# Performance work log

Hardware: AMD Instinct MI355X
Metric: run time of the kernel (lower is better)

Reference implementation:

```python
import jax, jax.numpy as jnp
import numpy as np

B, T, N, L, D, F = 8, 1024, 512, 4096, 512, 64  # batch, target, nodes, leaves, d_model, d_feature
BR = L // N  # branching factor: leaves per node


def setup_inputs() -> dict:
    key = jax.random.key(0)
    ks = jax.random.split(key, 10)
    s = 0.02
    return {
        "root": jax.random.normal(ks[0], (B, 1, F), dtype=jnp.float32),
        "node": jax.random.normal(ks[1], (B, N, D), dtype=jnp.float32),
        "leaf": jax.random.normal(ks[2], (B, L, D), dtype=jnp.float32),
        "target": jax.random.normal(ks[3], (B, T, D), dtype=jnp.float32),
        "Wq": jax.random.normal(ks[4], (D, F), dtype=jnp.float32) * s,
        "bq": jnp.zeros((F,), dtype=jnp.float32),
        "Wk": jax.random.normal(ks[5], (D, F), dtype=jnp.float32) * s,
        "bk": jnp.zeros((F,), dtype=jnp.float32),
        "Wv": jax.random.normal(ks[6], (D, F), dtype=jnp.float32) * s,
        "bv": jnp.zeros((F,), dtype=jnp.float32),
        "Wagg": jax.random.normal(ks[7], (D, 1), dtype=jnp.float32) * s,
        "bagg": jnp.zeros((1,), dtype=jnp.float32),
    }


def reference(root, node, leaf, target, Wq, bq, Wk, bk, Wv, bv, Wagg, bagg):
    # Shared DecoderLinear projections (same weights used for node and leaf).
    q = target @ Wq + bq                      # [B,T,F]
    node_k = node @ Wk + bk                   # [B,N,F]
    node_v = node @ Wv + bv                   # [B,N,F]
    leaf_k = leaf @ Wk + bk                   # [B,L,F]
    leaf_v = leaf @ Wv + bv                   # [B,L,F]

    scale = 1.0 / jnp.sqrt(jnp.asarray(F, dtype=q.dtype))
    # Dual-key attention weights (no value-matmul inside attention()).
    Aqn = jax.nn.softmax(jnp.einsum('btf,bnf->btn', q, node_k) * scale, axis=-1)  # [B,T,N]
    Aql = jax.nn.softmax(jnp.einsum('btf,blf->btl', q, leaf_k) * scale, axis=-1)  # [B,T,L]

    # Tree interpolation: each leaf mixes root, its parent node value, and itself.
    node_rep = jnp.repeat(node_v, BR, axis=1)               # [B,L,F]
    interp = (root + node_rep + leaf_v) / 3.0               # [B,L,F]

    # Upward cumulative aggregation: suffix mean along the leaf dimension.
    rev_cumsum = jnp.cumsum(interp[:, ::-1, :], axis=1)[:, ::-1, :]  # [B,L,F]
    counts = (L - jnp.arange(L)).astype(interp.dtype)[None, :, None]
    upward = rev_cumsum / counts                                     # [B,L,F]

    # Weighted aggregation: learned softmax weights over each node's leaf group.
    w = jax.nn.softmax((leaf @ Wagg + bagg).reshape(B, N, BR), axis=-1)   # [B,N,BR]
    node_hat = jnp.einsum('bnc,bncf->bnf', w, upward.reshape(B, N, BR, F))  # [B,N,F]

    # Fused cat + matmul + softmax.
    A = jnp.concatenate([Aqn, Aql], axis=-1)          # [B,T,N+L]
    V = jnp.concatenate([node_hat, leaf_v], axis=-2)  # [B,N+L,F]
    return jax.nn.softmax(jnp.einsum('btm,bmf->btf', A, V), axis=-1)  # [B,T,F]
```

## Files before the change

kernel.cpp:

```cpp
#include <hip/hip_runtime.h>

#define B_ 8
#define T_ 1024
#define N_ 512
#define L_ 4096
#define D_ 512
#define F_ 64
#define SLICES 8
#define TPS 9
#define KSTR 72
#define XSTR 264

typedef __attribute__((ext_vector_type(8))) short short8;
typedef __attribute__((ext_vector_type(4))) float f32x4;

__device__ __forceinline__ unsigned short f2bf(float x){
    unsigned u = __builtin_bit_cast(unsigned, x);
    u += 0x7FFFu + ((u >> 16) & 1u);
    return (unsigned short)(u >> 16);
}
__device__ __forceinline__ unsigned pack_bf(float lo, float hi){
    return (unsigned)f2bf(lo) | ((unsigned)f2bf(hi) << 16);
}
__device__ __forceinline__ float bf2f(unsigned short s){
    return __builtin_bit_cast(float, ((unsigned)s) << 16);
}
__device__ __forceinline__ short8 frag_from4(unsigned d0, unsigned d1, unsigned d2, unsigned d3){
    union { unsigned u[4]; short8 s; } t;
    t.u[0] = d0; t.u[1] = d1; t.u[2] = d2; t.u[3] = d3;
    return t.s;
}

__global__ __launch_bounds__(64)
void prep_kernel(const float* __restrict__ Wq, const float* __restrict__ bq,
                 const float* __restrict__ Wk, const float* __restrict__ bk,
                 const float* __restrict__ Wv, const float* __restrict__ bv,
                 unsigned short* __restrict__ Wq_t, unsigned short* __restrict__ Wkv_t,
                 float* __restrict__ bq_s, float* __restrict__ bkv)
{
    const int n = blockIdx.x;
    const int lane = threadIdx.x;
    if (n == 192) {
        bq_s[lane]   = bq[lane] * 0.125f;
        bkv[lane]    = bk[lane];
        bkv[64+lane] = bv[lane];
        return;
    }
    const int d0 = lane * 8;
    unsigned short t[8];
    if (n < 64) {
        #pragma unroll
        for (int j = 0; j < 8; ++j) t[j] = f2bf(Wq[(size_t)(d0+j)*F_ + n] * 0.125f);
        *(uint4*)&Wq_t[(size_t)n*D_ + d0] = make_uint4(
            (unsigned)t[0]|((unsigned)t[1]<<16), (unsigned)t[2]|((unsigned)t[3]<<16),
            (unsigned)t[4]|((unsigned)t[5]<<16), (unsigned)t[6]|((unsigned)t[7]<<16));
    } else {
        const int nn  = n - 64;
        const float* W = (nn < 64) ? Wk : Wv;
        const int col = nn & 63;
        #pragma unroll
        for (int j = 0; j < 8; ++j) t[j] = f2bf(W[(size_t)(d0+j)*F_ + col]);
        *(uint4*)&Wkv_t[(size_t)nn*D_ + d0] = make_uint4(
            (unsigned)t[0]|((unsigned)t[1]<<16), (unsigned)t[2]|((unsigned)t[3]<<16),
            (unsigned)t[4]|((unsigned)t[5]<<16), (unsigned)t[6]|((unsigned)t[7]<<16));
    }
}

template<int MODE>
__device__ __forceinline__ void proj_body(
    int r0, unsigned short* Xs, unsigned short* Ws, unsigned short* Vt_lds,
    const float* __restrict__ X,
    const unsigned short* __restrict__ Wt,
    const float* __restrict__ bias,
    const float* __restrict__ Wagg, const float* __restrict__ bagg,
    unsigned short* __restrict__ outK, float* __restrict__ outVf,
    unsigned short* __restrict__ outVt, float* __restrict__ outAgg)
{
    constexpr int NPASS = (MODE == 0) ? 1 : 2;
    const int tid = threadIdx.x;
    const int l = tid & 63, c = l & 15, h = l >> 4;
    const int w  = tid >> 6;
    const int nt = w & 3;
    const int m  = w >> 2;

    f32x4 acc0 = {0,0,0,0};
    f32x4 acc1 = {0,0,0,0};
    float pa = 0.f;

    #pragma unroll
    for (int kc = 0; kc < 2; ++kc) {
        #pragma unroll
        for (int j = 0; j < 4; ++j) {
            const int s = tid + j * 1024;
            const int row = s >> 6, col = s & 63;
            const float4 v = *(const float4*)(X + (size_t)(r0+row)*D_ + kc*256 + col*4);
            *(uint2*)&Xs[row*XSTR + col*4] =
                make_uint2(pack_bf(v.x, v.y), pack_bf(v.z, v.w));
        }
        {
            const int r = tid >> 4, ch = tid & 15;
            #pragma unroll
            for (int j = 0; j < 2; ++j) {
                const int u = ch + j*16;
                *(uint4*)&Ws[r*XSTR + u*8] =
                    *(const uint4*)(Wt + (size_t)r*D_ + kc*256 + u*8);
            }
        }
        __syncthreads();

        #pragma unroll
        for (int kk = 0; kk < 8; ++kk) {
            const short8 bfr = *(const short8*)&Ws[(16*nt + c)*XSTR + kk*32 + 8*h];
            const short8 af  = *(const short8*)&Xs[(16*m  + c)*XSTR + kk*32 + 8*h];
            acc0 = __builtin_amdgcn_mfma_f32_16x16x32_bf16(af, bfr, acc0, 0,0,0);
        }
        __syncthreads();

        if constexpr (NPASS == 2) {
            {
                const int r = tid >> 4, ch = tid & 15;
                #pragma unroll
                for (int j = 0; j < 2; ++j) {
                    const int u = ch + j*16;
                    *(uint4*)&Ws[r*XSTR + u*8] =
                        *(const uint4*)(Wt + (size_t)(64 + r)*D_ + kc*256 + u*8);
                }
            }
            __syncthreads();
            #pragma unroll
            for (int kk = 0; kk < 8; ++kk) {
                const short8 bfr = *(const short8*)&Ws[(16*nt + c)*XSTR + kk*32 + 8*h];
                const short8 af  = *(const short8*)&Xs[(16*m  + c)*XSTR + kk*32 + 8*h];
                acc1 = __builtin_amdgcn_mfma_f32_16x16x32_bf16(af, bfr, acc1, 0,0,0);
            }
            if constexpr (MODE == 2) {
                const int row = tid >> 4, qd = tid & 15;
                const unsigned short* xr = &Xs[row*XSTR + qd*16];
                const float* wr = Wagg + kc*256 + qd*16;
                #pragma unroll
                for (int j = 0; j < 2; ++j) {
                    const short8 xv = *(const short8*)(xr + j*8);
                    const float4 wa0 = *(const float4*)(wr + j*8);
                    const float4 wa1 = *(const float4*)(wr + j*8 + 4);
                    pa += bf2f((unsigned short)xv[0])*wa0.x + bf2f((unsigned short)xv[1])*wa0.y
                        + bf2f((unsigned short)xv[2])*wa0.z + bf2f((unsigned short)xv[3])*wa0.w
                        + bf2f((unsigned short)xv[4])*wa1.x + bf2f((unsigned short)xv[5])*wa1.y
                        + bf2f((unsigned short)xv[6])*wa1.z + bf2f((unsigned short)xv[7])*wa1.w;
                }
            }
            __syncthreads();
        }
    }

    {
        const float bc0 = bias[16*nt + c];
        #pragma unroll
        for (int r = 0; r < 4; ++r) {
            const int row = r0 + 16*m + 4*h + r;
            outK[(size_t)row*F_ + 16*nt + c] = f2bf(acc0[r] + bc0);
        }
    }
    if constexpr (NPASS == 2) {
        const float bc1 = bias[64 + 16*nt + c];
        #pragma unroll
        for (int r = 0; r < 4; ++r) {
            const int row = r0 + 16*m + 4*h + r;
            const float v = acc1[r] + bc1;
            if constexpr (MODE == 1) {
                outVf[(size_t)row*F_ + 16*nt + c] = v;
            } else {
                Vt_lds[(16*nt + c)*72 + 16*m + 4*h + r] = f2bf(v);
            }
        }
    }

    if constexpr (MODE == 2) {
        {
            const int row = tid >> 4, qd = tid & 15;
            pa += __shfl_xor(pa, 1);
            pa += __shfl_xor(pa, 2);
            pa += __shfl_xor(pa, 4);
            pa += __shfl_xor(pa, 8);
            if (qd == 0) outAgg[r0 + row] = pa + bagg[0];
        }
        __syncthreads();
        {
            const int f = tid >> 4, seg = tid & 15;
            const int b = r0 >> 12, l0 = r0 & (L_ - 1);
            const uint2 a0 = *(const uint2*)&Vt_lds[f*72 + seg*4];
            *(uint2*)(outVt + ((size_t)(b*F_ + f))*L_ + l0 + seg*4) = a0;
        }
    }
}

__global__ __launch_bounds__(1024, 8)
void proj_all(const float* __restrict__ target, const float* __restrict__ node,
              const float* __restrict__ leaf,
              const unsigned short* __restrict__ Wq_t,
              const unsigned short* __restrict__ Wkv_t,
              const float* __restrict__ bq_s, const float* __restrict__ bkv,
              const float* __restrict__ Wagg, const float* __restrict__ bagg,
              unsigned short* __restrict__ q_bf, unsigned short* __restrict__ nk_bf,
              float* __restrict__ node_v, unsigned short* __restrict__ lk_bf,
              unsigned short* __restrict__ lvt, float* __restrict__ agg)
{
    __shared__ unsigned short Xs[64 * XSTR];
    __shared__ unsigned short Ws[64 * XSTR];
    __shared__ unsigned short Vt_lds[64 * 72];
    const int blk = blockIdx.x;
    if (blk < 512) {
        proj_body<2>(blk*64, Xs, Ws, Vt_lds, leaf, Wkv_t, bkv, Wagg, bagg,
                     lk_bf, nullptr, lvt, agg);
    } else if (blk < 640) {
        proj_body<0>((blk-512)*64, Xs, Ws, Vt_lds, target, Wq_t, bq_s, nullptr, nullptr,
                     q_bf, nullptr, nullptr, nullptr);
    } else {
        proj_body<1>((blk-640)*64, Xs, Ws, Vt_lds, node, Wkv_t, bkv, nullptr, nullptr,
                     nk_bf, node_v, nullptr, nullptr);
    }
}

__global__ __launch_bounds__(256)
void scan_nh_kernel(const unsigned short* __restrict__ lvt,
                    const float* __restrict__ node_v,
                    const float* __restrict__ root,
                    const float* __restrict__ agg,
                    unsigned short* __restrict__ nh_t)
{
    const int gtid = blockIdx.x * 256 + threadIdx.x;
    const int wv   = gtid >> 6;
    const int lane = threadIdx.x & 63;
    const int b = wv >> 6;
    const int f = wv & 63;

    const unsigned short* vt = lvt + ((size_t)(b*F_ + f))*L_ + lane*64;
    const float rootf = root[b*F_ + f];
    short8 xv[8]; float nv[8]; float gv[8];
    #pragma unroll
    for (int g = 0; g < 8; ++g) {
        xv[g] = *(const short8*)(vt + g*8);
        nv[g] = node_v[((size_t)(b*N_ + lane*8 + g))*F_ + f];
        float s8 = 0.f;
        #pragma unroll
        for (int j = 0; j < 8; ++j) s8 += bf2f((unsigned short)xv[g][j]);
        gv[g] = (s8 + 8.f*(rootf + nv[g])) * (1.f/3.f);
    }

    float s[9];
    s[8] = 0.f;
    #pragma unroll
    for (int j = 7; j >= 0; --j) s[j] = s[j+1] + gv[j];

    float x = s[0];
    const float lsum = x;
    #pragma unroll
    for (int off = 1; off < 64; off <<= 1) {
        float t = __shfl_down(x, off);
        if (lane + off < 64) x += t;
    }
    const float excl = x - lsum;

    const float* aggb = agg + (size_t)b*L_ + lane*64;
    unsigned short out8[8];
    #pragma unroll
    for (int g = 0; g < 8; ++g) {
        const float4 a0 = *(const float4*)(aggb + g*8);
        const float4 a1 = *(const float4*)(aggb + g*8 + 4);
        const float av[8] = {a0.x,a0.y,a0.z,a0.w, a1.x,a1.y,a1.z,a1.w};
        float mx = av[0];
        #pragma unroll
        for (int cc = 1; cc < 8; ++cc) mx = fmaxf(mx, av[cc]);
        float wgt[8]; float wsum = 0.f;
        #pragma unroll
        for (int cc = 0; cc < 8; ++cc) { wgt[cc] = __expf(av[cc] - mx); wsum += wgt[cc]; }

        const float tn = excl + s[g+1];
        float run = 0.f, acc = 0.f;
        #pragma unroll
        for (int cc = 7; cc >= 0; --cc) {
            const int ll = lane*64 + g*8 + cc;
            const float interp = (rootf + nv[g] + bf2f((unsigned short)xv[g][cc])) * (1.f/3.f);
            run += interp;
            const float up = (tn + run) / (float)(L_ - ll);
            acc = fmaf(wgt[cc], up, acc);
        }
        out8[g] = f2bf(acc / wsum);
    }
    *(uint4*)&nh_t[((size_t)(b*F_ + f))*N_ + lane*8] = *(const uint4*)out8;
}

__global__ __launch_bounds__(512, 4)
void attn_kernel(const unsigned short* __restrict__ qb,
                 const unsigned short* __restrict__ nk,
                 const unsigned short* __restrict__ nht,
                 const unsigned short* __restrict__ lk,
                 const unsigned short* __restrict__ lvt,
                 unsigned short* __restrict__ pacc, float* __restrict__ pd)
{
    __shared__ unsigned short Ks[2][64*KSTR];
    __shared__ unsigned short Vt[2][64*KSTR];

    const int wg  = (blockIdx.x & 7) * 64 + (blockIdx.x >> 3);
    const int b   = wg >> 6;
    const int sl  = (wg >> 3) & 7;
    const int t0  = (wg & 7) * 128;

    const int tid = threadIdx.x;
    const int w   = tid >> 6;
    const int l   = tid & 63;
    const int c   = l & 15;
    const int h   = l >> 4;
    const int sm  = tid >> 3;
    const int sc  = tid & 7;

    const unsigned short* qrow = qb + ((size_t)(b*T_ + t0 + w*16 + c))*F_ + 8*h;
    const short8 qf0 = *(const short8*)qrow;
    const short8 qf1 = *(const short8*)(qrow + 32);

    f32x4 accN[4] = {{0,0,0,0},{0,0,0,0},{0,0,0,0},{0,0,0,0}};
    f32x4 accL[4] = {{0,0,0,0},{0,0,0,0},{0,0,0,0},{0,0,0,0}};
    float dsN = 0.f, dsL = 0.f;

    const unsigned short* Knb = nk  + (size_t)b*N_*F_;
    const unsigned short* Klb = lk  + (size_t)b*L_*F_;
    const unsigned short* Vnb = nht + (size_t)b*F_*N_;
    const unsigned short* Vlb = lvt + (size_t)b*F_*L_;

    const int ti0 = sl * TPS;

    uint4 sk0, sv0;
    auto load_tile = [&](int ti) {
        if (ti < 8) {
            sk0 = *(const uint4*)(Knb + (size_t)ti*64*F_ + sm*64 + sc*8);
            sv0 = *(const uint4*)(Vnb + (size_t)sm*N_ + ti*64 + sc*8);
        } else {
            sk0 = *(const uint4*)(Klb + (size_t)(ti-8)*64*F_ + sm*64 + sc*8);
            sv0 = *(const uint4*)(Vlb + (size_t)sm*L_ + (ti-8)*64 + sc*8);
        }
    };
    auto write_tile = [&](int pb) {
        *(uint4*)&Ks[pb][sm*KSTR + sc*8] = sk0;
        *(uint4*)&Vt[pb][sm*KSTR + sc*8] = sv0;
    };

    load_tile(ti0);
    write_tile(0);
    __syncthreads();

    const int srcA = c + 16*((2*h) & 3);
    const int srcB = c + 16*((2*h + 1) & 3);
    const int hs   = h >> 1;

    for (int i = 0; i < TPS; ++i) {
        const int  ti  = ti0 + i;
        const bool isN = ti < 8;
        const int  pb  = i & 1;
        const bool nxt = (i + 1 < TPS);
        if (nxt) load_tile(ti + 1);

        f32x4 st[4] = {{0,0,0,0},{0,0,0,0},{0,0,0,0},{0,0,0,0}};
        #pragma unroll
        for (int ss = 0; ss < 4; ++ss) {
            const short8 kf0 = *(const short8*)&Ks[pb][(16*ss + c)*KSTR + 8*h];
            st[ss] = __builtin_amdgcn_mfma_f32_16x16x32_bf16(kf0, qf0, st[ss], 0,0,0);
            const short8 kf1 = *(const short8*)&Ks[pb][(16*ss + c)*KSTR + 32 + 8*h];
            st[ss] = __builtin_amdgcn_mfma_f32_16x16x32_bf16(kf1, qf1, st[ss], 0,0,0);
        }

        unsigned pk0[4], pk1[4];
        float psum = 0.f;
        #pragma unroll
        for (int ss = 0; ss < 4; ++ss) {
            #pragma unroll
            for (int r = 0; r < 4; ++r) { st[ss][r] = __expf(st[ss][r]); psum += st[ss][r]; }
            pk0[ss] = pack_bf(st[ss][0], st[ss][1]);
            pk1[ss] = pack_bf(st[ss][2], st[ss][3]);
        }
        if (isN) dsN += psum; else dsL += psum;

        #pragma unroll
        for (int k00 = 0; k00 < 2; ++k00) {
            const unsigned d0a = __shfl(pk0[2*k00+0], srcA);
            const unsigned d0b = __shfl(pk0[2*k00+1], srcA);
            const unsigned d1a = __shfl(pk1[2*k00+0], srcA);
            const unsigned d1b = __shfl(pk1[2*k00+1], srcA);
            const unsigned d2a = __shfl(pk0[2*k00+0], srcB);
            const unsigned d2b = __shfl(pk0[2*k00+1], srcB);
            const unsigned d3a = __shfl(pk1[2*k00+0], srcB);
            const unsigned d3b = __shfl(pk1[2*k00+1], srcB);
            const short8 bp = frag_from4(hs ? d0b : d0a, hs ? d1b : d1a,
                                         hs ? d2b : d2a, hs ? d3b : d3a);
            if (isN) {
                #pragma unroll
                for (int s2 = 0; s2 < 4; ++s2) {
                    const short8 af = *(const short8*)&Vt[pb][(16*s2 + c)*KSTR + 32*k00 + 8*h];
                    accN[s2] = __builtin_amdgcn_mfma_f32_16x16x32_bf16(af, bp, accN[s2], 0,0,0);
                }
            } else {
                #pragma unroll
                for (int s2 = 0; s2 < 4; ++s2) {
                    const short8 af = *(const short8*)&Vt[pb][(16*s2 + c)*KSTR + 32*k00 + 8*h];
                    accL[s2] = __builtin_amdgcn_mfma_f32_16x16x32_bf16(af, bp, accL[s2], 0,0,0);
                }
            }
        }

        if (nxt) {
            write_tile(pb ^ 1);
            __syncthreads();
        }
    }

    dsN += __shfl_xor(dsN, 16);  dsN += __shfl_xor(dsN, 32);
    dsL += __shfl_xor(dsL, 16);  dsL += __shfl_xor(dsL, 32);

    const int gt = b*T_ + t0 + w*16 + c;
    unsigned short* baseN = pacc + (((size_t)sl*(B_*T_) + gt)*2 + 0)*F_;
    unsigned short* baseL = baseN + F_;
    #pragma unroll
    for (int s2 = 0; s2 < 4; ++s2) {
        *(unsigned*)&baseN[s2*16 + 4*h]     = pack_bf(accN[s2][0], accN[s2][1]);
        *(unsigned*)&baseN[s2*16 + 4*h + 2] = pack_bf(accN[s2][2], accN[s2][3]);
        *(unsigned*)&baseL[s2*16 + 4*h]     = pack_bf(accL[s2][0], accL[s2][1]);
        *(unsigned*)&baseL[s2*16 + 4*h + 2] = pack_bf(accL[s2][2], accL[s2][3]);
    }
    if (h == 0) {
        pd[((size_t)sl*(B_*T_) + gt)*2 + 0] = dsN;
        pd[((size_t)sl*(B_*T_) + gt)*2 + 1] = dsL;
    }
}

__global__ __launch_bounds__(256)
void combine_kernel(const unsigned short* __restrict__ pacc,
                    const float* __restrict__ pd,
                    float* __restrict__ out)
{
    const int gt = (blockIdx.x * 256 + threadIdx.x) >> 6;
    const int f  = threadIdx.x & 63;

    float aN = 0.f, aL = 0.f, dN = 0.f, dL = 0.f;
    #pragma unroll
    for (int s = 0; s < SLICES; ++s) {
        const size_t base = ((size_t)s*(B_*T_) + gt)*2;
        aN += bf2f(pacc[(base + 0)*F_ + f]);
        aL += bf2f(pacc[(base + 1)*F_ + f]);
        dN += pd[base + 0];
        dL += pd[base + 1];
    }
    float lg = aN / dN + aL / dL;
    float mx = lg;
    #pragma unroll
    for (int off = 1; off < 64; off <<= 1) mx = fmaxf(mx, __shfl_xor(mx, off));
    const float e = __expf(lg - mx);
    float ssum = e;
    #pragma unroll
    for (int off = 1; off < 64; off <<= 1) ssum += __shfl_xor(ssum, off);
    out[(size_t)gt*F_ + f] = e / ssum;
}

extern "C" void kernel_launch(void* const* d_in, const int* in_sizes, int n_in,
                              void* d_out, int out_size, void* d_ws, size_t ws_size,
                              hipStream_t stream)
{
    const float* root   = (const float*)d_in[0];
    const float* node   = (const float*)d_in[1];
    const float* leaf   = (const float*)d_in[2];
    const float* target = (const float*)d_in[3];
    const float* Wq   = (const float*)d_in[4];
    const float* bq   = (const float*)d_in[5];
    const float* Wk   = (const float*)d_in[6];
    const float* bk   = (const float*)d_in[7];
    const float* Wv   = (const float*)d_in[8];
    const float* bv   = (const float*)d_in[9];
    const float* Wagg = (const float*)d_in[10];
    const float* bagg = (const float*)d_in[11];
    float* out = (float*)d_out;

    char* wp = (char*)d_ws;
    unsigned short* q_bf  = (unsigned short*)wp; wp += (size_t)B_*T_*F_*2;
    unsigned short* nk_bf = (unsigned short*)wp; wp += (size_t)B_*N_*F_*2;
    unsigned short* lk_bf = (unsigned short*)wp; wp += (size_t)B_*L_*F_*2;
    unsigned short* lvt   = (unsigned short*)wp; wp += (size_t)B_*F_*L_*2;
    unsigned short* nht   = (unsigned short*)wp; wp += (size_t)B_*F_*N_*2;
    unsigned short* Wq_t  = (unsigned short*)wp; wp += (size_t)64*D_*2;
    unsigned short* Wkv_t = (unsigned short*)wp; wp += (size_t)128*D_*2;
    float* node_v = (float*)wp; wp += (size_t)B_*N_*F_*4;
    float* agg    = (float*)wp; wp += (size_t)B_*L_*4;
    float* bq_s   = (float*)wp; wp += 512;
    float* bkv    = (float*)wp; wp += 512;
    unsigned short* pacc = (unsigned short*)wp; wp += (size_t)SLICES*B_*T_*2*F_*2;
    float* pd     = (float*)wp;

    prep_kernel<<<193, 64, 0, stream>>>(Wq, bq, Wk, bk, Wv, bv, Wq_t, Wkv_t, bq_s, bkv);
    proj_all<<<704, 1024, 0, stream>>>(target, node, leaf, Wq_t, Wkv_t, bq_s, bkv,
                                       Wagg, bagg, q_bf, nk_bf, node_v, lk_bf, lvt, agg);
    scan_nh_kernel<<<128, 256, 0, stream>>>(lvt, node_v, root, agg, nht);
    attn_kernel<<<B_*(T_/128)*SLICES, 512, 0, stream>>>(q_bf, nk_bf, nht, lk_bf, lvt, pacc, pd);
    combine_kernel<<<(B_*T_)/4, 256, 0, stream>>>(pacc, pd, out);
}
```

Measured before the change: 78.78 us.

## Double-buffer projection LDS tiles and prefetch next K-chunk during MFMA

The projection kernel now splits D into four 128-wide chunks with ping-pong LDS buffers for both X and W. The next chunk's global loads are issued into registers before the MFMA loop and stored to LDS afterward, so there is one barrier per phase instead of two or three. The Wagg dot product is moved out of the LDS path and recomputed in fp32 from global memory after the main loop. This rereads leaf rows from global/L2, and the extra registers from the prefetch may lower occupancy at 1024 threads per block.

```diff
diff --git a/kernel.cpp b/kernel.cpp
--- a/kernel.cpp
+++ b/kernel.cpp
@@ -9,7 +9,7 @@
 #define SLICES 8
 #define TPS 9
 #define KSTR 72
-#define XSTR 264
+#define PSTR 136
 
 typedef __attribute__((ext_vector_type(8))) short short8;
 typedef __attribute__((ext_vector_type(4))) float f32x4;
@@ -68,7 +68,10 @@
 
 template<int MODE>
 __device__ __forceinline__ void proj_body(
-    int r0, unsigned short* Xs, unsigned short* Ws, unsigned short* Vt_lds,
+    int r0,
+    unsigned short* Xs0, unsigned short* Xs1,
+    unsigned short* Ws0, unsigned short* Ws1,
+    unsigned short* Vt_lds,
     const float* __restrict__ X,
     const unsigned short* __restrict__ Wt,
     const float* __restrict__ bias,
@@ -76,77 +79,68 @@
     unsigned short* __restrict__ outK, float* __restrict__ outVf,
     unsigned short* __restrict__ outVt, float* __restrict__ outAgg)
 {
-    constexpr int NPASS = (MODE == 0) ? 1 : 2;
+    constexpr int NP = (MODE == 0) ? 1 : 2;
+    constexpr int PH = 4 * NP;
     const int tid = threadIdx.x;
     const int l = tid & 63, c = l & 15, h = l >> 4;
     const int w  = tid >> 6;
     const int nt = w & 3;
     const int m  = w >> 2;
 
+    const int wr = tid >> 4, wch = tid & 15;
+    const int xs0i = tid, xs1i = tid + 1024;
+
+    {
+        const float4 a = *(const float4*)(X + (size_t)(r0 + (xs0i >> 5))*D_ + (xs0i & 31)*4);
+        const float4 b = *(const float4*)(X + (size_t)(r0 + (xs1i >> 5))*D_ + (xs1i & 31)*4);
+        *(uint2*)&Xs0[(xs0i >> 5)*PSTR + (xs0i & 31)*4] =
+            make_uint2(pack_bf(a.x, a.y), pack_bf(a.z, a.w));
+        *(uint2*)&Xs0[(xs1i >> 5)*PSTR + (xs1i & 31)*4] =
+            make_uint2(pack_bf(b.x, b.y), pack_bf(b.z, b.w));
+        *(uint4*)&Ws0[wr*PSTR + wch*8] = *(const uint4*)(Wt + (size_t)wr*D_ + wch*8);
+    }
+    __syncthreads();
+
     f32x4 acc0 = {0,0,0,0};
     f32x4 acc1 = {0,0,0,0};
-    float pa = 0.f;
-
-    #pragma unroll
-    for (int kc = 0; kc < 2; ++kc) {
-        #pragma unroll
-        for (int j = 0; j < 4; ++j) {
-            const int s = tid + j * 1024;
-            const int row = s >> 6, col = s & 63;
-            const float4 v = *(const float4*)(X + (size_t)(r0+row)*D_ + kc*256 + col*4);
-            *(uint2*)&Xs[row*XSTR + col*4] =
-                make_uint2(pack_bf(v.x, v.y), pack_bf(v.z, v.w));
-        }
-        {
-            const int r = tid >> 4, ch = tid & 15;
-            #pragma unroll
-            for (int j = 0; j < 2; ++j) {
-                const int u = ch + j*16;
-                *(uint4*)&Ws[r*XSTR + u*8] =
-                    *(const uint4*)(Wt + (size_t)r*D_ + kc*256 + u*8);
+
+    #pragma unroll
+    for (int ph = 0; ph < PH; ++ph) {
+        const int kc  = ph / NP;
+        const int p   = ph % NP;
+        const bool nxt = (ph + 1 < PH);
+        const int kc2 = (ph + 1) / NP;
+        const int p2  = (ph + 1) % NP;
+
+        uint4 wreg;
+        float4 xa, xb;
+        if (nxt) {
+            wreg = *(const uint4*)(Wt + (size_t)(64*p2 + wr)*D_ + kc2*128 + wch*8);
+            if (kc2 != kc) {
+                xa = *(const float4*)(X + (size_t)(r0 + (xs0i >> 5))*D_ + kc2*128 + (xs0i & 31)*4);
+                xb = *(const float4*)(X + (size_t)(r0 + (xs1i >> 5))*D_ + kc2*128 + (xs1i & 31)*4);
             }
         }
-        __syncthreads();
-
-        #pragma unroll
-        for (int kk = 0; kk < 8; ++kk) {
-            const short8 bfr = *(const short8*)&Ws[(16*nt + c)*XSTR + kk*32 + 8*h];
-            const short8 af  = *(const short8*)&Xs[(16*m  + c)*XSTR + kk*32 + 8*h];
-            acc0 = __builtin_amdgcn_mfma_f32_16x16x32_bf16(af, bfr, acc0, 0,0,0);
-        }
-        __syncthreads();
-
-        if constexpr (NPASS == 2) {
-            {
-                const int r = tid >> 4, ch = tid & 15;
-                #pragma unroll
-                for (int j = 0; j < 2; ++j) {
-                    const int u = ch + j*16;
-                    *(uint4*)&Ws[r*XSTR + u*8] =
-                        *(const uint4*)(Wt + (size_t)(64 + r)*D_ + kc*256 + u*8);
-                }
-            }
-            __syncthreads();
-            #pragma unroll
-            for (int kk = 0; kk < 8; ++kk) {
-                const short8 bfr = *(const short8*)&Ws[(16*nt + c)*XSTR + kk*32 + 8*h];
-                const short8 af  = *(const short8*)&Xs[(16*m  + c)*XSTR + kk*32 + 8*h];
-                acc1 = __builtin_amdgcn_mfma_f32_16x16x32_bf16(af, bfr, acc1, 0,0,0);
-            }
-            if constexpr (MODE == 2) {
-                const int row = tid >> 4, qd = tid & 15;
-                const unsigned short* xr = &Xs[row*XSTR + qd*16];
-                const float* wr = Wagg + kc*256 + qd*16;
-                #pragma unroll
-                for (int j = 0; j < 2; ++j) {
-                    const short8 xv = *(const short8*)(xr + j*8);
-                    const float4 wa0 = *(const float4*)(wr + j*8);
-                    const float4 wa1 = *(const float4*)(wr + j*8 + 4);
-                    pa += bf2f((unsigned short)xv[0])*wa0.x + bf2f((unsigned short)xv[1])*wa0.y
-                        + bf2f((unsigned short)xv[2])*wa0.z + bf2f((unsigned short)xv[3])*wa0.w
-                        + bf2f((unsigned short)xv[4])*wa1.x + bf2f((unsigned short)xv[5])*wa1.y
-                        + bf2f((unsigned short)xv[6])*wa1.z + bf2f((unsigned short)xv[7])*wa1.w;
-                }
+
+        const unsigned short* Wc = (ph & 1) ? Ws1 : Ws0;
+        const unsigned short* Xc = (kc & 1) ? Xs1 : Xs0;
+        #pragma unroll
+        for (int kk = 0; kk < 4; ++kk) {
+            const short8 bfr = *(const short8*)&Wc[(16*nt + c)*PSTR + kk*32 + 8*h];
+            const short8 af  = *(const short8*)&Xc[(16*m  + c)*PSTR + kk*32 + 8*h];
+            if (p == 0) acc0 = __builtin_amdgcn_mfma_f32_16x16x32_bf16(af, bfr, acc0, 0,0,0);
+            else        acc1 = __builtin_amdgcn_mfma_f32_16x16x32_bf16(af, bfr, acc1, 0,0,0);
+        }
+
+        if (nxt) {
+            unsigned short* Wn = (ph & 1) ? Ws0 : Ws1;
+            *(uint4*)&Wn[wr*PSTR + wch*8] = wreg;
+            if (kc2 != kc) {
+                unsigned short* Xn = (kc & 1) ? Xs0 : Xs1;
+                *(uint2*)&Xn[(xs0i >> 5)*PSTR + (xs0i & 31)*4] =
+                    make_uint2(pack_bf(xa.x, xa.y), pack_bf(xa.z, xa.w));
+                *(uint2*)&Xn[(xs1i >> 5)*PSTR + (xs1i & 31)*4] =
+                    make_uint2(pack_bf(xb.x, xb.y), pack_bf(xb.z, xb.w));
             }
             __syncthreads();
         }
@@ -160,7 +154,7 @@
             outK[(size_t)row*F_ + 16*nt + c] = f2bf(acc0[r] + bc0);
         }
     }
-    if constexpr (NPASS == 2) {
+    if constexpr (NP == 2) {
         const float bc1 = bias[64 + 16*nt + c];
         #pragma unroll
         for (int r = 0; r < 4; ++r) {
@@ -177,6 +171,15 @@
     if constexpr (MODE == 2) {
         {
             const int row = tid >> 4, qd = tid & 15;
+            const float* xr = X + (size_t)(r0 + row)*D_ + qd*32;
+            const float* wrg = Wagg + qd*32;
+            float pa = 0.f;
+            #pragma unroll
+            for (int j = 0; j < 8; ++j) {
+                const float4 xv = *(const float4*)(xr + j*4);
+                const float4 wa = *(const float4*)(wrg + j*4);
+                pa += xv.x*wa.x + xv.y*wa.y + xv.z*wa.z + xv.w*wa.w;
+            }
             pa += __shfl_xor(pa, 1);
             pa += __shfl_xor(pa, 2);
             pa += __shfl_xor(pa, 4);
@@ -204,19 +207,21 @@
               float* __restrict__ node_v, unsigned short* __restrict__ lk_bf,
               unsigned short* __restrict__ lvt, float* __restrict__ agg)
 {
-    __shared__ unsigned short Xs[64 * XSTR];
-    __shared__ unsigned short Ws[64 * XSTR];
+    __shared__ unsigned short Xs0[64 * PSTR];
+    __shared__ unsigned short Xs1[64 * PSTR];
+    __shared__ unsigned short Ws0[64 * PSTR];
+    __shared__ unsigned short Ws1[64 * PSTR];
     __shared__ unsigned short Vt_lds[64 * 72];
     const int blk = blockIdx.x;
     if (blk < 512) {
-        proj_body<2>(blk*64, Xs, Ws, Vt_lds, leaf, Wkv_t, bkv, Wagg, bagg,
-                     lk_bf, nullptr, lvt, agg);
+        proj_body<2>(blk*64, Xs0, Xs1, Ws0, Ws1, Vt_lds, leaf, Wkv_t, bkv,
+                     Wagg, bagg, lk_bf, nullptr, lvt, agg);
     } else if (blk < 640) {
-        proj_body<0>((blk-512)*64, Xs, Ws, Vt_lds, target, Wq_t, bq_s, nullptr, nullptr,
-                     q_bf, nullptr, nullptr, nullptr);
+        proj_body<0>((blk-512)*64, Xs0, Xs1, Ws0, Ws1, Vt_lds, target, Wq_t, bq_s,
+                     nullptr, nullptr, q_bf, nullptr, nullptr, nullptr);
     } else {
-        proj_body<1>((blk-640)*64, Xs, Ws, Vt_lds, node, Wkv_t, bkv, nullptr, nullptr,
-                     nk_bf, node_v, nullptr, nullptr);
+        proj_body<1>((blk-640)*64, Xs0, Xs1, Ws0, Ws1, Vt_lds, node, Wkv_t, bkv,
+                     nullptr, nullptr, nk_bf, node_v, nullptr, nullptr);
     }
 }
 
```

New measurement: 89.54 us. +13.7%, slower.

## Prefetch projection inputs and weights into registers ahead of LDS compute

Applied to the files above, without the earlier changes.

The projection body now issues all global loads of the X tile (both K halves) up front into registers, and prefetches the next weight chunk into registers while the current MFMA loop runs. The fixed two-iteration K loop is unrolled into an explicit staged schedule, so global memory latency overlaps with matrix compute instead of sitting between barriers. The cost is much higher register pressure from holding eight float4 plus weight registers per thread, which may reduce occupancy.

```diff
diff --git a/kernel.cpp b/kernel.cpp
--- a/kernel.cpp
+++ b/kernel.cpp
@@ -82,74 +82,101 @@
     const int w  = tid >> 6;
     const int nt = w & 3;
     const int m  = w >> 2;
+    const int wr = tid >> 4, wch = tid & 15;
+
+    float4 xr0[4], xr1[4];
+    #pragma unroll
+    for (int j = 0; j < 4; ++j) {
+        const int s = tid + j*1024, row = s >> 6, col = s & 63;
+        xr0[j] = *(const float4*)(X + (size_t)(r0+row)*D_ + col*4);
+    }
+    #pragma unroll
+    for (int j = 0; j < 4; ++j) {
+        const int s = tid + j*1024, row = s >> 6, col = s & 63;
+        xr1[j] = *(const float4*)(X + (size_t)(r0+row)*D_ + 256 + col*4);
+    }
+    uint4 wreg[2];
+    #pragma unroll
+    for (int j = 0; j < 2; ++j)
+        wreg[j] = *(const uint4*)(Wt + (size_t)wr*D_ + (wch + j*16)*8);
 
     f32x4 acc0 = {0,0,0,0};
     f32x4 acc1 = {0,0,0,0};
     float pa = 0.f;
 
-    #pragma unroll
-    for (int kc = 0; kc < 2; ++kc) {
+    auto writeX = [&](const float4* xr) {
         #pragma unroll
         for (int j = 0; j < 4; ++j) {
-            const int s = tid + j * 1024;
-            const int row = s >> 6, col = s & 63;
-            const float4 v = *(const float4*)(X + (size_t)(r0+row)*D_ + kc*256 + col*4);
+            const int s = tid + j*1024, row = s >> 6, col = s & 63;
             *(uint2*)&Xs[row*XSTR + col*4] =
-                make_uint2(pack_bf(v.x, v.y), pack_bf(v.z, v.w));
-        }
-        {
-            const int r = tid >> 4, ch = tid & 15;
-            #pragma unroll
-            for (int j = 0; j < 2; ++j) {
-                const int u = ch + j*16;
-                *(uint4*)&Ws[r*XSTR + u*8] =
-                    *(const uint4*)(Wt + (size_t)r*D_ + kc*256 + u*8);
-            }
-        }
-        __syncthreads();
-
+                make_uint2(pack_bf(xr[j].x, xr[j].y), pack_bf(xr[j].z, xr[j].w));
+        }
+    };
+    auto writeW = [&]() {
+        #pragma unroll
+        for (int j = 0; j < 2; ++j)
+            *(uint4*)&Ws[wr*XSTR + (wch + j*16)*8] = wreg[j];
+    };
+    auto issueW = [&](int p, int kc) {
+        #pragma unroll
+        for (int j = 0; j < 2; ++j)
+            wreg[j] = *(const uint4*)(Wt + (size_t)(64*p + wr)*D_ + kc*256 + (wch + j*16)*8);
+    };
+    auto compute = [&](f32x4& acc) {
         #pragma unroll
         for (int kk = 0; kk < 8; ++kk) {
             const short8 bfr = *(const short8*)&Ws[(16*nt + c)*XSTR + kk*32 + 8*h];
             const short8 af  = *(const short8*)&Xs[(16*m  + c)*XSTR + kk*32 + 8*h];
-            acc0 = __builtin_amdgcn_mfma_f32_16x16x32_bf16(af, bfr, acc0, 0,0,0);
-        }
-        __syncthreads();
-
-        if constexpr (NPASS == 2) {
-            {
-                const int r = tid >> 4, ch = tid & 15;
-                #pragma unroll
-                for (int j = 0; j < 2; ++j) {
-                    const int u = ch + j*16;
-                    *(uint4*)&Ws[r*XSTR + u*8] =
-                        *(const uint4*)(Wt + (size_t)(64 + r)*D_ + kc*256 + u*8);
-                }
-            }
-            __syncthreads();
-            #pragma unroll
-            for (int kk = 0; kk < 8; ++kk) {
-                const short8 bfr = *(const short8*)&Ws[(16*nt + c)*XSTR + kk*32 + 8*h];
-                const short8 af  = *(const short8*)&Xs[(16*m  + c)*XSTR + kk*32 + 8*h];
-                acc1 = __builtin_amdgcn_mfma_f32_16x16x32_bf16(af, bfr, acc1, 0,0,0);
-            }
-            if constexpr (MODE == 2) {
-                const int row = tid >> 4, qd = tid & 15;
-                const unsigned short* xr = &Xs[row*XSTR + qd*16];
-                const float* wr = Wagg + kc*256 + qd*16;
-                #pragma unroll
-                for (int j = 0; j < 2; ++j) {
-                    const short8 xv = *(const short8*)(xr + j*8);
-                    const float4 wa0 = *(const float4*)(wr + j*8);
-                    const float4 wa1 = *(const float4*)(wr + j*8 + 4);
-                    pa += bf2f((unsigned short)xv[0])*wa0.x + bf2f((unsigned short)xv[1])*wa0.y
-                        + bf2f((unsigned short)xv[2])*wa0.z + bf2f((unsigned short)xv[3])*wa0.w
-                        + bf2f((unsigned short)xv[4])*wa1.x + bf2f((unsigned short)xv[5])*wa1.y
-                        + bf2f((unsigned short)xv[6])*wa1.z + bf2f((unsigned short)xv[7])*wa1.w;
-                }
-            }
-            __syncthreads();
-        }
+            acc = __builtin_amdgcn_mfma_f32_16x16x32_bf16(af, bfr, acc, 0,0,0);
+        }
+    };
+    auto aggpart = [&](int kc) {
+        const int row = tid >> 4, qd = tid & 15;
+        const unsigned short* xr = &Xs[row*XSTR + qd*16];
+        const float* wrg = Wagg + kc*256 + qd*16;
+        #pragma unroll
+        for (int j = 0; j < 2; ++j) {
+            const short8 xv = *(const short8*)(xr + j*8);
+            const float4 wa0 = *(const float4*)(wrg + j*8);
+            const float4 wa1 = *(const float4*)(wrg + j*8 + 4);
+            pa += bf2f((unsigned short)xv[0])*wa0.x + bf2f((unsigned short)xv[1])*wa0.y
+                + bf2f((unsigned short)xv[2])*wa0.z + bf2f((unsigned short)xv[3])*wa0.w
+                + bf2f((unsigned short)xv[4])*wa1.x + bf2f((unsigned short)xv[5])*wa1.y
+                + bf2f((unsigned short)xv[6])*wa1.z + bf2f((unsigned short)xv[7])*wa1.w;
+        }
+    };
+
+    writeX(xr0);
+    writeW();
+    __syncthreads();
+    if constexpr (NPASS == 2) {
+        issueW(1, 0);
+        compute(acc0);
+        __syncthreads();
+        writeW();
+        __syncthreads();
+        issueW(0, 1);
+        compute(acc1);
+        if constexpr (MODE == 2) aggpart(0);
+        __syncthreads();
+    } else {
+        issueW(0, 1);
+        compute(acc0);
+        __syncthreads();
+    }
+    writeX(xr1);
+    writeW();
+    __syncthreads();
+    if constexpr (NPASS == 2) {
+        issueW(1, 1);
+        compute(acc0);
+        __syncthreads();
+        writeW();
+        __syncthreads();
+        compute(acc1);
+        if constexpr (MODE == 2) aggpart(1);
+    } else {
+        compute(acc0);
     }
 
     {
```

After: 94.70 us. 1.2x slower.

## Halve projection block size, compute two row tiles per wave, smaller K chunks

Applied to the files above, without the earlier changes.

The projection kernel moves from 1024 to 512 threads per block. Each wave now computes two 16-row M tiles and reuses one B fragment across both. The K dimension is staged in four 128-wide chunks instead of two 256-wide ones, which shrinks LDS per block and should let more blocks fit on each CU. The transposed V store is widened to 16-byte writes. In exchange there are more barriers per block and more accumulators per thread.

```diff
diff --git a/kernel.cpp b/kernel.cpp
--- a/kernel.cpp
+++ b/kernel.cpp
@@ -9,7 +9,7 @@
 #define SLICES 8
 #define TPS 9
 #define KSTR 72
-#define XSTR 264
+#define PSTR 136
 
 typedef __attribute__((ext_vector_type(8))) short short8;
 typedef __attribute__((ext_vector_type(4))) float f32x4;
@@ -81,62 +81,63 @@
     const int l = tid & 63, c = l & 15, h = l >> 4;
     const int w  = tid >> 6;
     const int nt = w & 3;
-    const int m  = w >> 2;
-
-    f32x4 acc0 = {0,0,0,0};
-    f32x4 acc1 = {0,0,0,0};
+    const int m0 = (w >> 2) * 2;
+    const int m1 = m0 + 1;
+
+    f32x4 aK0 = {0,0,0,0}, aK1 = {0,0,0,0};
+    f32x4 aV0 = {0,0,0,0}, aV1 = {0,0,0,0};
     float pa = 0.f;
 
     #pragma unroll
-    for (int kc = 0; kc < 2; ++kc) {
+    for (int kc = 0; kc < 4; ++kc) {
         #pragma unroll
         for (int j = 0; j < 4; ++j) {
-            const int s = tid + j * 1024;
-            const int row = s >> 6, col = s & 63;
-            const float4 v = *(const float4*)(X + (size_t)(r0+row)*D_ + kc*256 + col*4);
-            *(uint2*)&Xs[row*XSTR + col*4] =
+            const int s = tid + j * 512;
+            const int row = s >> 5, col = s & 31;
+            const float4 v = *(const float4*)(X + (size_t)(r0+row)*D_ + kc*128 + col*4);
+            *(uint2*)&Xs[row*PSTR + col*4] =
                 make_uint2(pack_bf(v.x, v.y), pack_bf(v.z, v.w));
         }
-        {
-            const int r = tid >> 4, ch = tid & 15;
+        #pragma unroll
+        for (int j = 0; j < 2; ++j) {
+            const int s = tid + j * 512;
+            const int row = s >> 4, ch = s & 15;
+            *(uint4*)&Ws[row*PSTR + ch*8] =
+                *(const uint4*)(Wt + (size_t)row*D_ + kc*128 + ch*8);
+        }
+        __syncthreads();
+
+        #pragma unroll
+        for (int kk = 0; kk < 4; ++kk) {
+            const short8 bfr = *(const short8*)&Ws[(16*nt + c)*PSTR + kk*32 + 8*h];
+            const short8 a0  = *(const short8*)&Xs[(16*m0 + c)*PSTR + kk*32 + 8*h];
+            const short8 a1  = *(const short8*)&Xs[(16*m1 + c)*PSTR + kk*32 + 8*h];
+            aK0 = __builtin_amdgcn_mfma_f32_16x16x32_bf16(a0, bfr, aK0, 0,0,0);
+            aK1 = __builtin_amdgcn_mfma_f32_16x16x32_bf16(a1, bfr, aK1, 0,0,0);
+        }
+        __syncthreads();
+
+        if constexpr (NPASS == 2) {
             #pragma unroll
             for (int j = 0; j < 2; ++j) {
-                const int u = ch + j*16;
-                *(uint4*)&Ws[r*XSTR + u*8] =
-                    *(const uint4*)(Wt + (size_t)r*D_ + kc*256 + u*8);
-            }
-        }
-        __syncthreads();
-
-        #pragma unroll
-        for (int kk = 0; kk < 8; ++kk) {
-            const short8 bfr = *(const short8*)&Ws[(16*nt + c)*XSTR + kk*32 + 8*h];
-            const short8 af  = *(const short8*)&Xs[(16*m  + c)*XSTR + kk*32 + 8*h];
-            acc0 = __builtin_amdgcn_mfma_f32_16x16x32_bf16(af, bfr, acc0, 0,0,0);
-        }
-        __syncthreads();
-
-        if constexpr (NPASS == 2) {
-            {
-                const int r = tid >> 4, ch = tid & 15;
-                #pragma unroll
-                for (int j = 0; j < 2; ++j) {
-                    const int u = ch + j*16;
-                    *(uint4*)&Ws[r*XSTR + u*8] =
-                        *(const uint4*)(Wt + (size_t)(64 + r)*D_ + kc*256 + u*8);
-                }
+                const int s = tid + j * 512;
+                const int row = s >> 4, ch = s & 15;
+                *(uint4*)&Ws[row*PSTR + ch*8] =
+                    *(const uint4*)(Wt + (size_t)(64 + row)*D_ + kc*128 + ch*8);
             }
             __syncthreads();
             #pragma unroll
-            for (int kk = 0; kk < 8; ++kk) {
-                const short8 bfr = *(const short8*)&Ws[(16*nt + c)*XSTR + kk*32 + 8*h];
-                const short8 af  = *(const short8*)&Xs[(16*m  + c)*XSTR + kk*32 + 8*h];
-                acc1 = __builtin_amdgcn_mfma_f32_16x16x32_bf16(af, bfr, acc1, 0,0,0);
+            for (int kk = 0; kk < 4; ++kk) {
+                const short8 bfr = *(const short8*)&Ws[(16*nt + c)*PSTR + kk*32 + 8*h];
+                const short8 a0  = *(const short8*)&Xs[(16*m0 + c)*PSTR + kk*32 + 8*h];
+                const short8 a1  = *(const short8*)&Xs[(16*m1 + c)*PSTR + kk*32 + 8*h];
+                aV0 = __builtin_amdgcn_mfma_f32_16x16x32_bf16(a0, bfr, aV0, 0,0,0);
+                aV1 = __builtin_amdgcn_mfma_f32_16x16x32_bf16(a1, bfr, aV1, 0,0,0);
             }
             if constexpr (MODE == 2) {
-                const int row = tid >> 4, qd = tid & 15;
-                const unsigned short* xr = &Xs[row*XSTR + qd*16];
-                const float* wr = Wagg + kc*256 + qd*16;
+                const int row = tid >> 3, qd = tid & 7;
+                const unsigned short* xr = &Xs[row*PSTR + qd*16];
+                const float* wr = Wagg + kc*128 + qd*16;
                 #pragma unroll
                 for (int j = 0; j < 2; ++j) {
                     const short8 xv = *(const short8*)(xr + j*8);
@@ -156,44 +157,49 @@
         const float bc0 = bias[16*nt + c];
         #pragma unroll
         for (int r = 0; r < 4; ++r) {
-            const int row = r0 + 16*m + 4*h + r;
-            outK[(size_t)row*F_ + 16*nt + c] = f2bf(acc0[r] + bc0);
+            const int rowA = r0 + 16*m0 + 4*h + r;
+            const int rowB = r0 + 16*m1 + 4*h + r;
+            outK[(size_t)rowA*F_ + 16*nt + c] = f2bf(aK0[r] + bc0);
+            outK[(size_t)rowB*F_ + 16*nt + c] = f2bf(aK1[r] + bc0);
         }
     }
     if constexpr (NPASS == 2) {
         const float bc1 = bias[64 + 16*nt + c];
         #pragma unroll
         for (int r = 0; r < 4; ++r) {
-            const int row = r0 + 16*m + 4*h + r;
-            const float v = acc1[r] + bc1;
+            const int rowA = r0 + 16*m0 + 4*h + r;
+            const int rowB = r0 + 16*m1 + 4*h + r;
+            const float v0 = aV0[r] + bc1;
+            const float v1 = aV1[r] + bc1;
             if constexpr (MODE == 1) {
-                outVf[(size_t)row*F_ + 16*nt + c] = v;
+                outVf[(size_t)rowA*F_ + 16*nt + c] = v0;
+                outVf[(size_t)rowB*F_ + 16*nt + c] = v1;
             } else {
-                Vt_lds[(16*nt + c)*72 + 16*m + 4*h + r] = f2bf(v);
+                Vt_lds[(16*nt + c)*72 + 16*m0 + 4*h + r] = f2bf(v0);
+                Vt_lds[(16*nt + c)*72 + 16*m1 + 4*h + r] = f2bf(v1);
             }
         }
     }
 
     if constexpr (MODE == 2) {
         {
-            const int row = tid >> 4, qd = tid & 15;
+            const int row = tid >> 3, qd = tid & 7;
             pa += __shfl_xor(pa, 1);
             pa += __shfl_xor(pa, 2);
             pa += __shfl_xor(pa, 4);
-            pa += __shfl_xor(pa, 8);
             if (qd == 0) outAgg[r0 + row] = pa + bagg[0];
         }
         __syncthreads();
         {
-            const int f = tid >> 4, seg = tid & 15;
+            const int f = tid >> 3, seg = tid & 7;
             const int b = r0 >> 12, l0 = r0 & (L_ - 1);
-            const uint2 a0 = *(const uint2*)&Vt_lds[f*72 + seg*4];
-            *(uint2*)(outVt + ((size_t)(b*F_ + f))*L_ + l0 + seg*4) = a0;
-        }
-    }
-}
-
-__global__ __launch_bounds__(1024, 8)
+            const uint4 a0 = *(const uint4*)&Vt_lds[f*72 + seg*8];
+            *(uint4*)(outVt + ((size_t)(b*F_ + f))*L_ + l0 + seg*8) = a0;
+        }
+    }
+}
+
+__global__ __launch_bounds__(512, 6)
 void proj_all(const float* __restrict__ target, const float* __restrict__ node,
               const float* __restrict__ leaf,
               const unsigned short* __restrict__ Wq_t,
@@ -204,8 +210,8 @@
               float* __restrict__ node_v, unsigned short* __restrict__ lk_bf,
               unsigned short* __restrict__ lvt, float* __restrict__ agg)
 {
-    __shared__ unsigned short Xs[64 * XSTR];
-    __shared__ unsigned short Ws[64 * XSTR];
+    __shared__ unsigned short Xs[64 * PSTR];
+    __shared__ unsigned short Ws[64 * PSTR];
     __shared__ unsigned short Vt_lds[64 * 72];
     const int blk = blockIdx.x;
     if (blk < 512) {
@@ -492,8 +498,8 @@
     float* pd     = (float*)wp;
 
     prep_kernel<<<193, 64, 0, stream>>>(Wq, bq, Wk, bk, Wv, bv, Wq_t, Wkv_t, bq_s, bkv);
-    proj_all<<<704, 1024, 0, stream>>>(target, node, leaf, Wq_t, Wkv_t, bq_s, bkv,
-                                       Wagg, bagg, q_bf, nk_bf, node_v, lk_bf, lvt, agg);
+    proj_all<<<704, 512, 0, stream>>>(target, node, leaf, Wq_t, Wkv_t, bq_s, bkv,
+                                      Wagg, bagg, q_bf, nk_bf, node_v, lk_bf, lvt, agg);
     scan_nh_kernel<<<128, 256, 0, stream>>>(lvt, node_v, root, agg, nht);
     attn_kernel<<<B_*(T_/128)*SLICES, 512, 0, stream>>>(q_bf, nk_bf, nht, lk_bf, lvt, pacc, pd);
     combine_kernel<<<(B_*T_)/4, 256, 0, stream>>>(pacc, pd, out);
```

Result: slower. 98.97 us (+25.6%).
